# Kernel optimization log

Measured on AMD Instinct MI355X. Metric: run time of the kernel, lower is better.

Reference implementation:

```python
import jax, jax.numpy as jnp
import numpy as np


def setup_inputs() -> dict:
    key = jax.random.key(0)
    x = jax.random.normal(key, (4096, 512), dtype=jnp.float32)
    return {"x": x}


def reference(x):
    # Pairwise Euclidean distances for all (i, j) with i > j, flattened in the
    # same order as the original nested loop: (1,0),(2,0),(2,1),(3,0),...
    n = x.shape[0]
    sq = jnp.sum(x * x, axis=1)                      # [N]
    gram = x @ x.T                                   # [N, N]
    d2 = sq[:, None] + sq[None, :] - 2.0 * gram      # [N, N] squared dists
    ii, jj = jnp.tril_indices(n, k=-1)               # row-major lower triangle
    return jnp.sqrt(jnp.maximum(d2[ii, jj], 0.0))    # [N*(N-1)/2]
```

## Files before the change

kernel.cpp:

```cpp
#include <hip/hip_runtime.h>
#include <hip/hip_bf16.h>
#include <stdint.h>

#define N 4096
#define D 512
#define TILE 128
#define BK 32
#define KITERS (D / BK)
#define NB (N / TILE)

typedef __bf16 bf16x8 __attribute__((ext_vector_type(8)));
typedef float f32x4 __attribute__((ext_vector_type(4)));

__global__ __launch_bounds__(256) void prep_kernel(const float* __restrict__ x,
                                                   __bf16* __restrict__ xb,
                                                   float* __restrict__ sq) {
    int row  = blockIdx.x * 4 + (threadIdx.x >> 6);
    int lane = threadIdx.x & 63;
    const float* xr = x + (size_t)row * D + lane * 8;
    float4 v0 = *reinterpret_cast<const float4*>(xr);
    float4 v1 = *reinterpret_cast<const float4*>(xr + 4);

    bf16x8 b;
    b[0] = (__bf16)v0.x; b[1] = (__bf16)v0.y; b[2] = (__bf16)v0.z; b[3] = (__bf16)v0.w;
    b[4] = (__bf16)v1.x; b[5] = (__bf16)v1.y; b[6] = (__bf16)v1.z; b[7] = (__bf16)v1.w;
    *reinterpret_cast<bf16x8*>(xb + (size_t)row * D + lane * 8) = b;

    float s = v0.x * v0.x + v0.y * v0.y + v0.z * v0.z + v0.w * v0.w +
              v1.x * v1.x + v1.y * v1.y + v1.z * v1.z + v1.w * v1.w;
    #pragma unroll
    for (int off = 32; off > 0; off >>= 1) s += __shfl_down(s, off);
    if (lane == 0) sq[row] = s;
}

__global__ __launch_bounds__(256) void pairdist_kernel(const __bf16* __restrict__ xb,
                                                       const float* __restrict__ sq,
                                                       float* __restrict__ out) {
    __shared__ __bf16 As[2][TILE * BK];
    __shared__ __bf16 Bs[2][TILE * BK];

    int t  = blockIdx.x;
    int bi = (int)((sqrtf(8.0f * (float)t + 1.0f) - 1.0f) * 0.5f);
    while ((bi + 1) * (bi + 2) / 2 <= t) bi++;
    while (bi * (bi + 1) / 2 > t) bi--;
    int bj = t - bi * (bi + 1) / 2;

    int tid  = threadIdx.x;
    int w    = tid >> 6;
    int lane = tid & 63;
    int quad = lane >> 4;
    int lr   = lane & 15;
    int wm   = w >> 1;
    int wn   = w & 1;

    f32x4 acc[4][4];
    #pragma unroll
    for (int mt = 0; mt < 4; mt++)
        #pragma unroll
        for (int nt = 0; nt < 4; nt++)
            acc[mt][nt] = (f32x4)0.0f;

    int srow = lane >> 2;
    int scol = (lane & 3) * 8;
    const __bf16* ga = xb + (size_t)(bi * TILE + w * 16 + srow) * D + scol;
    const __bf16* gb = xb + (size_t)(bj * TILE + w * 16 + srow) * D + scol;
    int ldsoff = w * 16 * BK;

#define STAGE(buf, k0)                                                        \
    do {                                                                      \
        __builtin_amdgcn_global_load_lds(                                     \
            (const __attribute__((address_space(1))) void*)(ga + (k0)),       \
            (__attribute__((address_space(3))) void*)(As[buf] + ldsoff),      \
            16, 0, 0);                                                        \
        __builtin_amdgcn_global_load_lds(                                     \
            (const __attribute__((address_space(1))) void*)(ga + (k0) + (size_t)64 * D), \
            (__attribute__((address_space(3))) void*)(As[buf] + ldsoff + 64 * BK), \
            16, 0, 0);                                                        \
        __builtin_amdgcn_global_load_lds(                                     \
            (const __attribute__((address_space(1))) void*)(gb + (k0)),       \
            (__attribute__((address_space(3))) void*)(Bs[buf] + ldsoff),      \
            16, 0, 0);                                                        \
        __builtin_amdgcn_global_load_lds(                                     \
            (const __attribute__((address_space(1))) void*)(gb + (k0) + (size_t)64 * D), \
            (__attribute__((address_space(3))) void*)(Bs[buf] + ldsoff + 64 * BK), \
            16, 0, 0);                                                        \
    } while (0)

    STAGE(0, 0);
    __syncthreads();

    for (int it = 0; it < KITERS; ++it) {
        int cur = it & 1;
        if (it + 1 < KITERS) STAGE(cur ^ 1, (it + 1) * BK);

        bf16x8 af[4], bfr[4];
        #pragma unroll
        for (int mt = 0; mt < 4; mt++)
            af[mt] = *reinterpret_cast<const bf16x8*>(
                As[cur] + (wm * 64 + mt * 16 + lr) * BK + quad * 8);
        #pragma unroll
        for (int nt = 0; nt < 4; nt++)
            bfr[nt] = *reinterpret_cast<const bf16x8*>(
                Bs[cur] + (wn * 64 + nt * 16 + lr) * BK + quad * 8);

        #pragma unroll
        for (int mt = 0; mt < 4; mt++)
            #pragma unroll
            for (int nt = 0; nt < 4; nt++)
                acc[mt][nt] = __builtin_amdgcn_mfma_f32_16x16x32_bf16(
                    af[mt], bfr[nt], acc[mt][nt], 0, 0, 0);

        __syncthreads();
    }
#undef STAGE

    int ibase = bi * TILE + wm * 64;
    int jbase = bj * TILE + wn * 64;

    float sqi[4][4], sqj[4];
    #pragma unroll
    for (int mt = 0; mt < 4; mt++)
        #pragma unroll
        for (int tt = 0; tt < 4; tt++)
            sqi[mt][tt] = sq[ibase + mt * 16 + quad * 4 + tt];
    #pragma unroll
    for (int nt = 0; nt < 4; nt++)
        sqj[nt] = sq[jbase + nt * 16 + lr];

    if (bi != bj) {
        #pragma unroll
        for (int mt = 0; mt < 4; mt++) {
            #pragma unroll
            for (int tt = 0; tt < 4; tt++) {
                int i = ibase + mt * 16 + quad * 4 + tt;
                unsigned rowoff = (unsigned)(i * (i - 1) / 2);
                #pragma unroll
                for (int nt = 0; nt < 4; nt++) {
                    int j = jbase + nt * 16 + lr;
                    float d2 = sqi[mt][tt] + sqj[nt] - 2.0f * acc[mt][nt][tt];
                    out[rowoff + (unsigned)j] = sqrtf(fmaxf(d2, 0.0f));
                }
            }
        }
    } else {
        #pragma unroll
        for (int mt = 0; mt < 4; mt++) {
            #pragma unroll
            for (int tt = 0; tt < 4; tt++) {
                int i = ibase + mt * 16 + quad * 4 + tt;
                unsigned rowoff = (unsigned)(i * (i - 1) / 2);
                #pragma unroll
                for (int nt = 0; nt < 4; nt++) {
                    int j = jbase + nt * 16 + lr;
                    if (j < i) {
                        float d2 = sqi[mt][tt] + sqj[nt] - 2.0f * acc[mt][nt][tt];
                        out[rowoff + (unsigned)j] = sqrtf(fmaxf(d2, 0.0f));
                    }
                }
            }
        }
    }
}

extern "C" void kernel_launch(void* const* d_in, const int* in_sizes, int n_in,
                              void* d_out, int out_size, void* d_ws, size_t ws_size,
                              hipStream_t stream) {
    const float* x = (const float*)d_in[0];
    float* out = (float*)d_out;

    __bf16* xb = (__bf16*)d_ws;
    float* sq  = (float*)((char*)d_ws + (size_t)N * D * sizeof(__bf16));

    prep_kernel<<<N / 4, 256, 0, stream>>>(x, xb, sq);

    int nblocks = NB * (NB + 1) / 2;
    pairdist_kernel<<<nblocks, 256, 0, stream>>>(xb, sq, out);
}
```

Before: 99.38 us.

## Quantize inputs to FP8 and use scaled 16x16x128 MFMA with swizzled LDS

The prep kernel now packs the rows into FP8 (e4m3) instead of bf16. The Gram matmul uses the gfx950 scaled MFMA f8f6f4 16x16x128 instruction with unit scales, and the K tile grows to 128. The double-buffered LDS pipeline is replaced by a single buffer with an XOR-swizzled layout to avoid bank conflicts, and launch bounds are set for two blocks per CU. This halves operand bytes and MFMA issue count at the cost of lower precision in the dot products, which could hurt accuracy of the distances. Loads are no longer overlapped with compute.

After: 80.47 us. -19.0%, faster.

```diff
diff --git a/kernel.cpp b/kernel.cpp
--- a/kernel.cpp
+++ b/kernel.cpp
@@ -5,15 +5,16 @@
 #define N 4096
 #define D 512
 #define TILE 128
-#define BK 32
+#define BK 128
 #define KITERS (D / BK)
 #define NB (N / TILE)
 
-typedef __bf16 bf16x8 __attribute__((ext_vector_type(8)));
 typedef float f32x4 __attribute__((ext_vector_type(4)));
+typedef int   i32x8 __attribute__((ext_vector_type(8)));
+typedef int   i32x4 __attribute__((ext_vector_type(4)));
 
 __global__ __launch_bounds__(256) void prep_kernel(const float* __restrict__ x,
-                                                   __bf16* __restrict__ xb,
+                                                   unsigned char* __restrict__ xq,
                                                    float* __restrict__ sq) {
     int row  = blockIdx.x * 4 + (threadIdx.x >> 6);
     int lane = threadIdx.x & 63;
@@ -21,10 +22,11 @@
     float4 v0 = *reinterpret_cast<const float4*>(xr);
     float4 v1 = *reinterpret_cast<const float4*>(xr + 4);
 
-    bf16x8 b;
-    b[0] = (__bf16)v0.x; b[1] = (__bf16)v0.y; b[2] = (__bf16)v0.z; b[3] = (__bf16)v0.w;
-    b[4] = (__bf16)v1.x; b[5] = (__bf16)v1.y; b[6] = (__bf16)v1.z; b[7] = (__bf16)v1.w;
-    *reinterpret_cast<bf16x8*>(xb + (size_t)row * D + lane * 8) = b;
+    int w0 = __builtin_amdgcn_cvt_pk_fp8_f32(v0.x, v0.y, 0, false);
+    w0     = __builtin_amdgcn_cvt_pk_fp8_f32(v0.z, v0.w, w0, true);
+    int w1 = __builtin_amdgcn_cvt_pk_fp8_f32(v1.x, v1.y, 0, false);
+    w1     = __builtin_amdgcn_cvt_pk_fp8_f32(v1.z, v1.w, w1, true);
+    reinterpret_cast<int2*>(xq + (size_t)row * D)[lane] = make_int2(w0, w1);
 
     float s = v0.x * v0.x + v0.y * v0.y + v0.z * v0.z + v0.w * v0.w +
               v1.x * v1.x + v1.y * v1.y + v1.z * v1.z + v1.w * v1.w;
@@ -33,11 +35,11 @@
     if (lane == 0) sq[row] = s;
 }
 
-__global__ __launch_bounds__(256) void pairdist_kernel(const __bf16* __restrict__ xb,
-                                                       const float* __restrict__ sq,
-                                                       float* __restrict__ out) {
-    __shared__ __bf16 As[2][TILE * BK];
-    __shared__ __bf16 Bs[2][TILE * BK];
+__global__ __launch_bounds__(256, 2) void pairdist_kernel(const unsigned char* __restrict__ xq,
+                                                          const float* __restrict__ sq,
+                                                          float* __restrict__ out) {
+    __shared__ __align__(16) unsigned char As[TILE * BK];
+    __shared__ __align__(16) unsigned char Bs[TILE * BK];
 
     int t  = blockIdx.x;
     int bi = (int)((sqrtf(8.0f * (float)t + 1.0f) - 1.0f) * 0.5f);
@@ -60,59 +62,57 @@
         for (int nt = 0; nt < 4; nt++)
             acc[mt][nt] = (f32x4)0.0f;
 
-    int srow = lane >> 2;
-    int scol = (lane & 3) * 8;
-    const __bf16* ga = xb + (size_t)(bi * TILE + w * 16 + srow) * D + scol;
-    const __bf16* gb = xb + (size_t)(bj * TILE + w * 16 + srow) * D + scol;
-    int ldsoff = w * 16 * BK;
+    int srow   = lane >> 3;
+    int schunk = lane & 7;
+    int sw     = ((schunk ^ srow) << 4);
+    const unsigned char* ga = xq + (size_t)(bi * TILE + w * 32 + srow) * D + sw;
+    const unsigned char* gb = xq + (size_t)(bj * TILE + w * 32 + srow) * D + sw;
+    unsigned char* la = As + w * 32 * BK;
+    unsigned char* lb = Bs + w * 32 * BK;
 
-#define STAGE(buf, k0)                                                        \
-    do {                                                                      \
-        __builtin_amdgcn_global_load_lds(                                     \
-            (const __attribute__((address_space(1))) void*)(ga + (k0)),       \
-            (__attribute__((address_space(3))) void*)(As[buf] + ldsoff),      \
-            16, 0, 0);                                                        \
-        __builtin_amdgcn_global_load_lds(                                     \
-            (const __attribute__((address_space(1))) void*)(ga + (k0) + (size_t)64 * D), \
-            (__attribute__((address_space(3))) void*)(As[buf] + ldsoff + 64 * BK), \
-            16, 0, 0);                                                        \
-        __builtin_amdgcn_global_load_lds(                                     \
-            (const __attribute__((address_space(1))) void*)(gb + (k0)),       \
-            (__attribute__((address_space(3))) void*)(Bs[buf] + ldsoff),      \
-            16, 0, 0);                                                        \
-        __builtin_amdgcn_global_load_lds(                                     \
-            (const __attribute__((address_space(1))) void*)(gb + (k0) + (size_t)64 * D), \
-            (__attribute__((address_space(3))) void*)(Bs[buf] + ldsoff + 64 * BK), \
-            16, 0, 0);                                                        \
-    } while (0)
+    for (int k0 = 0; k0 < D; k0 += BK) {
+        __syncthreads();
+        #pragma unroll
+        for (int g = 0; g < 4; g++) {
+            __builtin_amdgcn_global_load_lds(
+                (const __attribute__((address_space(1))) void*)(ga + k0 + (size_t)g * 8 * D),
+                (__attribute__((address_space(3))) void*)(la + g * 8 * BK), 16, 0, 0);
+            __builtin_amdgcn_global_load_lds(
+                (const __attribute__((address_space(1))) void*)(gb + k0 + (size_t)g * 8 * D),
+                (__attribute__((address_space(3))) void*)(lb + g * 8 * BK), 16, 0, 0);
+        }
+        __syncthreads();
 
-    STAGE(0, 0);
-    __syncthreads();
-
-    for (int it = 0; it < KITERS; ++it) {
-        int cur = it & 1;
-        if (it + 1 < KITERS) STAGE(cur ^ 1, (it + 1) * BK);
-
-        bf16x8 af[4], bfr[4];
+        int c0 = (((2 * quad) ^ (lr & 7)) << 4);
+        int c1 = c0 ^ 16;
+        i32x8 af[4], bfr[4];
         #pragma unroll
-        for (int mt = 0; mt < 4; mt++)
-            af[mt] = *reinterpret_cast<const bf16x8*>(
-                As[cur] + (wm * 64 + mt * 16 + lr) * BK + quad * 8);
+        for (int mt = 0; mt < 4; mt++) {
+            const unsigned char* rb = As + (wm * 64 + mt * 16 + lr) * BK;
+            i32x4 lo = *reinterpret_cast<const i32x4*>(rb + c0);
+            i32x4 hi = *reinterpret_cast<const i32x4*>(rb + c1);
+            af[mt][0] = lo[0]; af[mt][1] = lo[1]; af[mt][2] = lo[2]; af[mt][3] = lo[3];
+            af[mt][4] = hi[0]; af[mt][5] = hi[1]; af[mt][6] = hi[2]; af[mt][7] = hi[3];
+        }
         #pragma unroll
-        for (int nt = 0; nt < 4; nt++)
-            bfr[nt] = *reinterpret_cast<const bf16x8*>(
-                Bs[cur] + (wn * 64 + nt * 16 + lr) * BK + quad * 8);
+        for (int nt = 0; nt < 4; nt++) {
+            const unsigned char* rb = Bs + (wn * 64 + nt * 16 + lr) * BK;
+            i32x4 lo = *reinterpret_cast<const i32x4*>(rb + c0);
+            i32x4 hi = *reinterpret_cast<const i32x4*>(rb + c1);
+            bfr[nt][0] = lo[0]; bfr[nt][1] = lo[1]; bfr[nt][2] = lo[2]; bfr[nt][3] = lo[3];
+            bfr[nt][4] = hi[0]; bfr[nt][5] = hi[1]; bfr[nt][6] = hi[2]; bfr[nt][7] = hi[3];
+        }
 
         #pragma unroll
         for (int mt = 0; mt < 4; mt++)
             #pragma unroll
             for (int nt = 0; nt < 4; nt++)
-                acc[mt][nt] = __builtin_amdgcn_mfma_f32_16x16x32_bf16(
-                    af[mt], bfr[nt], acc[mt][nt], 0, 0, 0);
-
-        __syncthreads();
+                acc[mt][nt] = __builtin_amdgcn_mfma_scale_f32_16x16x128_f8f6f4(
+                    af[mt], bfr[nt], acc[mt][nt],
+                    0, 0,
+                    0, 0x7F7F7F7F,
+                    0, 0x7F7F7F7F);
     }
-#undef STAGE
 
     int ibase = bi * TILE + wm * 64;
     int jbase = bj * TILE + wn * 64;
@@ -168,11 +168,11 @@
     const float* x = (const float*)d_in[0];
     float* out = (float*)d_out;
 
-    __bf16* xb = (__bf16*)d_ws;
-    float* sq  = (float*)((char*)d_ws + (size_t)N * D * sizeof(__bf16));
+    unsigned char* xq = (unsigned char*)d_ws;
+    float* sq = (float*)((char*)d_ws + (size_t)N * D);
 
-    prep_kernel<<<N / 4, 256, 0, stream>>>(x, xb, sq);
+    prep_kernel<<<N / 4, 256, 0, stream>>>(x, xq, sq);
 
     int nblocks = NB * (NB + 1) / 2;
-    pairdist_kernel<<<nblocks, 256, 0, stream>>>(xb, sq, out);
+    pairdist_kernel<<<nblocks, 256, 0, stream>>>(xq, sq, out);
 }
```
